# Kernel tuning notes

Measured on AMD Instinct MI355X. Metric: run time of the kernel, lower is better.

Reference implementation:

```python
import jax, jax.numpy as jnp
import numpy as np

B, T, I, H, O = 128, 2048, 128, 256, 128


def _lstm_step(h, c, x_t, wx, bx, wh, bh):
    # gates: [B, 4H], chunk order: input, forget, cell, output
    gates = x_t @ wx.T + bx + h @ wh.T + bh
    i_g, f_g, g_g, o_g = jnp.split(gates, 4, axis=1)
    i_t = jax.nn.sigmoid(i_g)
    f_t = jax.nn.sigmoid(f_g)
    g_t = jnp.tanh(g_g)
    o_t = jax.nn.sigmoid(o_g)
    cy = c * f_t + i_t * g_t
    hy = o_t * jnp.tanh(cy)
    return hy, cy


def _gru_step(h, x_t, wx, bx, wh, bh):
    # chunk order: reset, update, new
    x_g = x_t @ wx.T + bx
    h_g = h @ wh.T + bh
    x_r, x_z, x_n = jnp.split(x_g, 3, axis=1)
    h_r, h_z, h_n = jnp.split(h_g, 3, axis=1)
    r = jax.nn.sigmoid(x_r + h_r)
    z = jax.nn.sigmoid(x_z + h_z)
    n = jnp.tanh(x_n + r * h_n)
    return z * h + (1.0 - z) * n


def _run_direction(x_tbi, w1x, b1x, w1h, b1h, w2x, b2x, w2h, b2h):
    # x_tbi: [T, B, I]; returns final hidden of top cell [B, H]
    h1 = jnp.zeros((x_tbi.shape[1], H), x_tbi.dtype)
    c1 = jnp.zeros_like(h1)
    h2 = jnp.zeros_like(h1)

    def step(carry, x_t):
        h1, c1, h2 = carry
        h1, c1 = _lstm_step(h1, c1, x_t, w1x, b1x, w1h, b1h)
        h2 = _gru_step(h2, h1, w2x, b2x, w2h, b2h)
        return (h1, c1, h2), None

    (h1, c1, h2), _ = jax.lax.scan(step, (h1, c1, h2), x_tbi)
    return h2


def setup_inputs() -> dict:
    key = jax.random.key(0)
    ks = jax.random.split(key, 8)
    std1 = 1.0 / np.sqrt(H)
    u = lambda k, shape, s: jax.random.uniform(k, shape, jnp.float32, -s, s)
    x = jax.random.normal(ks[0], (B, T, I), jnp.float32)
    # Cell 1: LSTM(input=I, hidden=H)
    w1x = u(ks[1], (4 * H, I), std1)
    b1x = jnp.zeros((4 * H,), jnp.float32)
    w1h = u(ks[2], (4 * H, H), std1)
    b1h = jnp.zeros((4 * H,), jnp.float32)
    # Cell 2: GRU(input=H, hidden=H)
    w2x = u(ks[3], (3 * H, H), std1)
    b2x = jnp.zeros((3 * H,), jnp.float32)
    w2h = u(ks[4], (3 * H, H), std1)
    b2h = jnp.zeros((3 * H,), jnp.float32)
    # out_fc: Linear(2H -> O), kaiming-normal fan_in
    wo = jax.random.normal(ks[5], (O, 2 * H), jnp.float32) * np.sqrt(2.0 / (2 * H))
    bo = jnp.zeros((O,), jnp.float32)
    return {"x": x, "w1x": w1x, "b1x": b1x, "w1h": w1h, "b1h": b1h,
            "w2x": w2x, "b2x": b2x, "w2h": w2h, "b2h": b2h, "wo": wo, "bo": bo}


def reference(x, w1x, b1x, w1h, b1h, w2x, b2x, w2h, b2h, wo, bo):
    x_tbi = jnp.swapaxes(x, 0, 1)  # [T, B, I]
    h_fwd = _run_direction(x_tbi, w1x, b1x, w1h, b1h, w2x, b2x, w2h, b2h)
    h_bwd = _run_direction(x_tbi[::-1], w1x, b1x, w1h, b1h, w2x, b2x, w2h, b2h)
    h_cat = jnp.concatenate([h_fwd, h_bwd], axis=1)  # [B, 2H]
    return h_cat @ wo.T + bo  # [B, O]
```

## Files before the change

### kernel.cpp

```cpp
#include <hip/hip_runtime.h>

#define T_LEN 2048
#define I_DIM 128
#define H_DIM 256


#define XHI_OFF 0
#define XLO_OFF 8192
#define CRED_OFF 16384
#define HSTG_OFF 33280
#define LDS_BYTES 98304

typedef __attribute__((ext_vector_type(8))) short short8;
typedef __attribute__((ext_vector_type(16))) float f32x16;

__device__ __forceinline__ float sigmoidf_(float v) { return 1.f / (1.f + __expf(-v)); }
__device__ __forceinline__ float tanhf_fast(float v) {
    float t = __expf(-2.f * fabsf(v));
    float r = (1.f - t) / (1.f + t);
    return v < 0.f ? -r : r;
}
__device__ __forceinline__ unsigned short bf16_rne(float f) {
    unsigned u = __float_as_uint(f);
    return (unsigned short)((u + 0x7fffu + ((u >> 16) & 1u)) >> 16);
}
__device__ __forceinline__ void split2(float a, unsigned short& h, unsigned short& l) {
    h = bf16_rne(a);
    float hf = __uint_as_float(((unsigned)h) << 16);
    l = bf16_rne(a - hf);
}

__device__ __forceinline__ short8 ld_frag(const char* p) {
    union { unsigned long long u[2]; short8 s; } v;
    v.u[0] = __hip_atomic_load((const unsigned long long*)p,
                               __ATOMIC_RELAXED, __HIP_MEMORY_SCOPE_AGENT);
    v.u[1] = __hip_atomic_load((const unsigned long long*)(p + 8),
                               __ATOMIC_RELAXED, __HIP_MEMORY_SCOPE_AGENT);
    return v.s;
}

__device__ __forceinline__ void stage_x_fn(const float* __restrict__ x, char* smem_b,
                                           int b0, int teff, int tid) {
    int b = tid >> 3, cq = tid & 7;
    const float4* src = (const float4*)(x + ((size_t)(b0 + b) * T_LEN + teff) * I_DIM + cq * 16);
    float4 v0 = src[0], v1 = src[1], v2 = src[2], v3 = src[3];
    float f[16] = {v0.x, v0.y, v0.z, v0.w, v1.x, v1.y, v1.z, v1.w,
                   v2.x, v2.y, v2.z, v2.w, v3.x, v3.y, v3.z, v3.w};
    short8 H0, H1, L0, L1;
    #pragma unroll
    for (int e = 0; e < 8; ++e) {
        unsigned short h, l;
        split2(f[e], h, l);      H0[e] = (short)h; L0[e] = (short)l;
        split2(f[8 + e], h, l);  H1[e] = (short)h; L1[e] = (short)l;
    }
    char* base = smem_b + cq * 1024 + b * 16;
    *(short8*)(base + XHI_OFF)       = H0;
    *(short8*)(base + XHI_OFF + 512) = H1;
    *(short8*)(base + XLO_OFF)       = L0;
    *(short8*)(base + XLO_OFF + 512) = L1;
}

#define MFMA3(ac, ah, al, bh, bl)                                              \
    ac = __builtin_amdgcn_mfma_f32_32x32x16_bf16(ah, bh, ac, 0, 0, 0);         \
    ac = __builtin_amdgcn_mfma_f32_32x32x16_bf16(ah, bl, ac, 0, 0, 0);         \
    ac = __builtin_amdgcn_mfma_f32_32x32x16_bf16(al, bh, ac, 0, 0, 0);

#define ACCSEL(i) ((i & 3) == 0 ? acc0 : (i & 3) == 1 ? acc1 : (i & 3) == 2 ? acc2 : acc3)

__global__ __launch_bounds__(256, 1)
void brnn_persistent(const float* __restrict__ x,
                     const float* __restrict__ w1x, const float* __restrict__ b1x,
                     const float* __restrict__ w1h, const float* __restrict__ b1h,
                     const float* __restrict__ w2x, const float* __restrict__ b2x,
                     const float* __restrict__ w2h, const float* __restrict__ b2h,
                     int* flags, char* exgb, float* h2out)
{
    extern __shared__ char smem_b[];

    const int tid  = threadIdx.x;
    const int lane = tid & 63;
    const int wid  = tid >> 6;
    const int wg   = blockIdx.x;
    const int grp  = wg & 7;
    const int cu   = wg >> 3;
    const int dir  = grp >> 2;
    const int btile = grp & 3;
    const int b0   = btile * 32;

    const int nrow = lane & 31;
    const int jrow = nrow >> 2;
    const int q    = nrow & 3;
    const int half = lane >> 5;
    short8 BH[16], BL[16];
    {
        #pragma unroll
        for (int i = 0; i < 16; ++i) {
            short8 H, L;
            #pragma unroll
            for (int e = 0; e < 8; ++e) {
                int kk = i * 16 + half * 8 + e;
                float v = 0.f;
                if (wid == 0) {
                    if (i < 12) {
                        int k = kk;
                        int R = q * H_DIM + cu * 8 + jrow;
                        v = (k < I_DIM) ? w1x[R * I_DIM + k] : w1h[R * H_DIM + (k - I_DIM)];
                    }
                } else if (wid == 1) {
                    if (i < 12) {
                        int k = 192 + kk;
                        int R = q * H_DIM + cu * 8 + jrow;
                        v = w1h[R * H_DIM + (k - I_DIM)];
                    }
                } else if (wid == 2) {
                    if (q < 3) v = w2x[(q * H_DIM + cu * 8 + jrow) * H_DIM + kk];
                } else {
                    if (q == 0)      v = w2h[(0 * H_DIM + cu * 8 + jrow) * H_DIM + kk];
                    else if (q == 1) v = w2h[(1 * H_DIM + cu * 8 + jrow) * H_DIM + kk];
                    else if (q == 3) v = w2h[(2 * H_DIM + cu * 8 + jrow) * H_DIM + kk];
                }
                unsigned short hh, ll;
                split2(v, hh, ll);
                H[e] = (short)hh; L[e] = (short)ll;
            }
            BH[i] = H; BL[i] = L;
        }
    }

    const int bb = tid & 31;
    const int jj = tid >> 5;
    const float bi_ = b1x[0 * H_DIM + cu * 8 + jj] + b1h[0 * H_DIM + cu * 8 + jj];
    const float bf_ = b1x[1 * H_DIM + cu * 8 + jj] + b1h[1 * H_DIM + cu * 8 + jj];
    const float bg_ = b1x[2 * H_DIM + cu * 8 + jj] + b1h[2 * H_DIM + cu * 8 + jj];
    const float bo_ = b1x[3 * H_DIM + cu * 8 + jj] + b1h[3 * H_DIM + cu * 8 + jj];
    const float brz_r = b2x[0 * H_DIM + cu * 8 + jj] + b2h[0 * H_DIM + cu * 8 + jj];
    const float brz_z = b2x[1 * H_DIM + cu * 8 + jj] + b2h[1 * H_DIM + cu * 8 + jj];
    const float bnx_  = b2x[2 * H_DIM + cu * 8 + jj];
    const float bnh_  = b2h[2 * H_DIM + cu * 8 + jj];

    float c_reg = 0.f, h2_reg = 0.f;

    {
        char* p1 = exgb + (size_t)(1 * 8 + grp) * 65536;
        int off = (cu >> 1) * 1024 + (cu & 1) * 512;
        if (tid < 64) {
            __hip_atomic_store((unsigned long long*)(p1 + off + tid * 8), 0ull,
                               __ATOMIC_RELAXED, __HIP_MEMORY_SCOPE_AGENT);
            __hip_atomic_store((unsigned long long*)(p1 + 32768 + off + tid * 8), 0ull,
                               __ATOMIC_RELAXED, __HIP_MEMORY_SCOPE_AGENT);
        }
    }
    if (tid < 128) *(unsigned long long*)(smem_b + HSTG_OFF + 1024 + tid * 8) = 0ull;
    stage_x_fn(x, smem_b, b0, dir ? (T_LEN - 1) : 0, tid);
    __syncthreads();
    if (tid == 0)
        __hip_atomic_store(&flags[grp * 64 + cu], 1,
                           __ATOMIC_RELAXED, __HIP_MEMORY_SCOPE_AGENT);

    for (int s = 0; s <= T_LEN; ++s) {
        {
            int target = s + 1;
            if (tid < 64) {
                while (true) {
                    int v = (tid < 32)
                        ? __hip_atomic_load(&flags[grp * 64 + tid],
                                            __ATOMIC_RELAXED, __HIP_MEMORY_SCOPE_AGENT)
                        : 0x7fffffff;
                    if (__all(v >= target)) break;
                }
            }
            __syncthreads();
        }
        const char* exgR = exgb + (size_t)(((s + 1) & 1) * 8 + grp) * 65536;

        f32x16 acc0, acc1, acc2, acc3;
        #pragma unroll
        for (int r = 0; r < 16; ++r) { acc0[r] = 0.f; acc1[r] = 0.f; acc2[r] = 0.f; acc3[r] = 0.f; }

        if (wid == 0) {
            if (s < T_LEN) {
                short8 hA[4], lA[4];
                #pragma unroll
                for (int i = 0; i < 4; ++i) {
                    hA[i] = ld_frag(exgR + i * 1024 + lane * 16);
                    lA[i] = ld_frag(exgR + 32768 + i * 1024 + lane * 16);
                }
                #pragma unroll
                for (int i = 0; i < 8; ++i) {
                    short8 ah = *(const short8*)(smem_b + XHI_OFF + i * 1024 + lane * 16);
                    short8 al = *(const short8*)(smem_b + XLO_OFF + i * 1024 + lane * 16);
                    f32x16& ac = ACCSEL(i);
                    MFMA3(ac, ah, al, BH[i], BL[i]);
                }
                #pragma unroll
                for (int i = 0; i < 4; ++i) {
                    f32x16& ac = ACCSEL(8 + i);
                    MFMA3(ac, hA[i], lA[i], BH[8 + i], BL[8 + i]);
                }
            }
        } else if (wid == 1) {
            if (s < T_LEN) {
                short8 hA[12], lA[12];
                #pragma unroll
                for (int i = 0; i < 12; ++i) {
                    hA[i] = ld_frag(exgR + (4 + i) * 1024 + lane * 16);
                    lA[i] = ld_frag(exgR + 32768 + (4 + i) * 1024 + lane * 16);
                }
                #pragma unroll
                for (int i = 0; i < 12; ++i) {
                    f32x16& ac = ACCSEL(i);
                    MFMA3(ac, hA[i], lA[i], BH[i], BL[i]);
                }
            }
        } else {
            if (s >= 1) {
                const int sbase = (wid - 2) * 16;
                short8 hA[16], lA[16];
                #pragma unroll
                for (int i = 0; i < 16; ++i) {
                    hA[i] = ld_frag(exgR + (sbase + i) * 1024 + lane * 16);
                    lA[i] = ld_frag(exgR + 32768 + (sbase + i) * 1024 + lane * 16);
                }
                #pragma unroll
                for (int i = 0; i < 16; ++i) {
                    f32x16& ac = ACCSEL(i);
                    MFMA3(ac, hA[i], lA[i], BH[i], BL[i]);
                }
            }
        }
        {
            float* credw = (float*)(smem_b + CRED_OFF) + wid * 1056;
            #pragma unroll
            for (int r = 0; r < 16; ++r) {
                int b = (r & 3) + 8 * (r >> 2) + 4 * half;
                credw[nrow * 33 + b] = acc0[r] + acc1[r] + acc2[r] + acc3[r];
            }
        }
        __syncthreads();

        const float* cr = (const float*)(smem_b + CRED_OFF);
        #define CRD(w, g) cr[(w) * 1056 + (jj * 4 + (g)) * 33 + bb]
        if (s < T_LEN) {
            float gi = CRD(0, 0) + CRD(1, 0) + bi_;
            float gf = CRD(0, 1) + CRD(1, 1) + bf_;
            float gg = CRD(0, 2) + CRD(1, 2) + bg_;
            float go = CRD(0, 3) + CRD(1, 3) + bo_;
            float ig = sigmoidf_(gi), fg = sigmoidf_(gf);
            float cg = tanhf_fast(gg), og = sigmoidf_(go);
            c_reg = c_reg * fg + ig * cg;
            float h1v = og * tanhf_fast(c_reg);
            unsigned short h, l;
            split2(h1v, h, l);
            *(unsigned short*)(smem_b + HSTG_OFF + bb * 16 + jj * 2) = h;
            *(unsigned short*)(smem_b + HSTG_OFF + 512 + bb * 16 + jj * 2) = l;
        }
        if (s >= 1) {
            float rc = CRD(2, 0) + CRD(3, 0) + brz_r;
            float zc = CRD(2, 1) + CRD(3, 1) + brz_z;
            float xn = CRD(2, 2) + CRD(3, 2) + bnx_;
            float hn = CRD(2, 3) + CRD(3, 3) + bnh_;
            float rg = sigmoidf_(rc), zg = sigmoidf_(zc);
            float ng = tanhf_fast(xn + rg * hn);
            h2_reg = zg * h2_reg + (1.f - zg) * ng;
            if (s == T_LEN) {
                h2out[(size_t)(grp * 32 + bb) * H_DIM + cu * 8 + jj] = h2_reg;
            } else {
                unsigned short h, l;
                split2(h2_reg, h, l);
                *(unsigned short*)(smem_b + HSTG_OFF + 1024 + bb * 16 + jj * 2) = h;
                *(unsigned short*)(smem_b + HSTG_OFF + 1536 + bb * 16 + jj * 2) = l;
            }
        }
        #undef CRD
        __syncthreads();

        if (s == T_LEN) break;

        {
            char* exgW = exgb + (size_t)((s & 1) * 8 + grp) * 65536;
            unsigned long long v = *(const unsigned long long*)(smem_b + HSTG_OFF + tid * 8);
            int r = tid >> 6;
            int w = (tid & 63) * 8;
            int off = (r & 1) * 32768 + ((r >> 1) * 16 + (cu >> 1)) * 1024 + (cu & 1) * 512 + w;
            __hip_atomic_store((unsigned long long*)(exgW + off), v,
                               __ATOMIC_RELAXED, __HIP_MEMORY_SCOPE_AGENT);
        }
        __syncthreads();
        if (tid == 0)
            __hip_atomic_store(&flags[grp * 64 + cu], s + 2,
                               __ATOMIC_RELAXED, __HIP_MEMORY_SCOPE_AGENT);
        if (s + 1 < T_LEN)
            stage_x_fn(x, smem_b, b0, dir ? (T_LEN - 2 - s) : (s + 1), tid);
    }
}

__global__ __launch_bounds__(128)
void brnn_out(const float* __restrict__ h2out, const float* __restrict__ wo,
              const float* __restrict__ bo, float* __restrict__ out)
{
    __shared__ float hc[512];
    int b = blockIdx.x;
    int o = threadIdx.x;
    int btile = b >> 5, bi = b & 31;
    for (int k = threadIdx.x; k < 256; k += 128) {
        hc[k]       = h2out[((size_t)(btile)     * 32 + bi) * H_DIM + k];
        hc[256 + k] = h2out[((size_t)(4 + btile) * 32 + bi) * H_DIM + k];
    }
    __syncthreads();
    float acc = bo[o];
    const float4* w4 = (const float4*)&wo[(size_t)o * 512];
    #pragma unroll 8
    for (int k = 0; k < 128; ++k) {
        float4 w = w4[k];
        acc += w.x * hc[k * 4] + w.y * hc[k * 4 + 1] + w.z * hc[k * 4 + 2] + w.w * hc[k * 4 + 3];
    }
    out[b * 128 + o] = acc;
}

extern "C" void kernel_launch(void* const* d_in, const int* in_sizes, int n_in,
                              void* d_out, int out_size, void* d_ws, size_t ws_size,
                              hipStream_t stream) {
    const float* x   = (const float*)d_in[0];
    const float* w1x = (const float*)d_in[1];
    const float* b1x = (const float*)d_in[2];
    const float* w1h = (const float*)d_in[3];
    const float* b1h = (const float*)d_in[4];
    const float* w2x = (const float*)d_in[5];
    const float* b2x = (const float*)d_in[6];
    const float* w2h = (const float*)d_in[7];
    const float* b2h = (const float*)d_in[8];
    const float* wo  = (const float*)d_in[9];
    const float* bo  = (const float*)d_in[10];
    float* out = (float*)d_out;

    char* ws = (char*)d_ws;
    int* flags = (int*)ws;
    char* exgb = ws + 4096;
    float* h2out = (float*)(ws + 4096 + 1048576);

    hipMemsetAsync(flags, 0, 8 * 64 * sizeof(int), stream);

    size_t shmem = LDS_BYTES;
    hipFuncSetAttribute((const void*)brnn_persistent,
                        hipFuncAttributeMaxDynamicSharedMemorySize, (int)shmem);

    void* args[] = { (void*)&x, (void*)&w1x, (void*)&b1x, (void*)&w1h, (void*)&b1h,
                     (void*)&w2x, (void*)&b2x, (void*)&w2h, (void*)&b2h,
                     (void*)&flags, (void*)&exgb, (void*)&h2out };
    hipError_t err = hipLaunchCooperativeKernel((void*)brnn_persistent,
                                                dim3(256), dim3(256), args,
                                                (unsigned int)shmem, stream);
    if (err != hipSuccess) {
        brnn_persistent<<<dim3(256), dim3(256), shmem, stream>>>(
            x, w1x, b1x, w1h, b1h, w2x, b2x, w2h, b2h, flags, exgb, h2out);
    }

    brnn_out<<<dim3(128), dim3(128), 0, stream>>>(h2out, wo, bo, out);
}
```

Measured before the change: 13.01 ms.

## Decouple LSTM and GRU warp pairs with separate flags and intra-block barriers

Splits each block into an LSTM half and a GRU half. Each half has its own LDS spin barrier and its own global progress flag, so the GRU half can lag the LSTM by one step instead of both marching in lockstep under __syncthreads. Hidden states are written straight to the global exchange buffer from the pointwise threads, which removes the staging copy and an extra block barrier. The x input is prefetched two steps ahead into a triple buffer by one LSTM warp. The cost is extra polling of two flag arrays, spin barriers built on LDS atomics, and more complex ordering that could introduce races.

```diff
diff --git a/kernel.cpp b/kernel.cpp
--- a/kernel.cpp
+++ b/kernel.cpp
@@ -5,10 +5,9 @@
 #define H_DIM 256
 
 
-#define XHI_OFF 0
-#define XLO_OFF 8192
-#define CRED_OFF 16384
-#define HSTG_OFF 33280
+#define XB(p)    ((p) * 16384)
+#define CRED_OFF 49152
+#define BAR_OFF  66048
 #define LDS_BYTES 98304
 
 typedef __attribute__((ext_vector_type(8))) short short8;
@@ -29,7 +28,6 @@
     float hf = __uint_as_float(((unsigned)h) << 16);
     l = bf16_rne(a - hf);
 }
-
 __device__ __forceinline__ short8 ld_frag(const char* p) {
     union { unsigned long long u[2]; short8 s; } v;
     v.u[0] = __hip_atomic_load((const unsigned long long*)p,
@@ -38,10 +36,14 @@
                                __ATOMIC_RELAXED, __HIP_MEMORY_SCOPE_AGENT);
     return v.s;
 }
-
-__device__ __forceinline__ void stage_x_fn(const float* __restrict__ x, char* smem_b,
-                                           int b0, int teff, int tid) {
-    int b = tid >> 3, cq = tid & 7;
+__device__ __forceinline__ void pair_bar(int* c, int target) {
+    __threadfence_block();
+    __hip_atomic_fetch_add(c, 1, __ATOMIC_RELAXED, __HIP_MEMORY_SCOPE_WORKGROUP);
+    while (__hip_atomic_load(c, __ATOMIC_RELAXED, __HIP_MEMORY_SCOPE_WORKGROUP) < target) {}
+}
+
+__device__ __forceinline__ void stage_unit(const float* __restrict__ x, char* hi, char* lo,
+                                           int b0, int teff, int b, int cq) {
     const float4* src = (const float4*)(x + ((size_t)(b0 + b) * T_LEN + teff) * I_DIM + cq * 16);
     float4 v0 = src[0], v1 = src[1], v2 = src[2], v3 = src[3];
     float f[16] = {v0.x, v0.y, v0.z, v0.w, v1.x, v1.y, v1.z, v1.w,
@@ -53,11 +55,10 @@
         split2(f[e], h, l);      H0[e] = (short)h; L0[e] = (short)l;
         split2(f[8 + e], h, l);  H1[e] = (short)h; L1[e] = (short)l;
     }
-    char* base = smem_b + cq * 1024 + b * 16;
-    *(short8*)(base + XHI_OFF)       = H0;
-    *(short8*)(base + XHI_OFF + 512) = H1;
-    *(short8*)(base + XLO_OFF)       = L0;
-    *(short8*)(base + XLO_OFF + 512) = L1;
+    char* bh = hi + cq * 1024 + b * 16;
+    char* bl = lo + cq * 1024 + b * 16;
+    *(short8*)bh = H0; *(short8*)(bh + 512) = H1;
+    *(short8*)bl = L0; *(short8*)(bl + 512) = L1;
 }
 
 #define MFMA3(ac, ah, al, bh, bl)                                              \
@@ -127,105 +128,124 @@
         }
     }
 
-    const int bb = tid & 31;
-    const int jj = tid >> 5;
-    const float bi_ = b1x[0 * H_DIM + cu * 8 + jj] + b1h[0 * H_DIM + cu * 8 + jj];
-    const float bf_ = b1x[1 * H_DIM + cu * 8 + jj] + b1h[1 * H_DIM + cu * 8 + jj];
-    const float bg_ = b1x[2 * H_DIM + cu * 8 + jj] + b1h[2 * H_DIM + cu * 8 + jj];
-    const float bo_ = b1x[3 * H_DIM + cu * 8 + jj] + b1h[3 * H_DIM + cu * 8 + jj];
-    const float brz_r = b2x[0 * H_DIM + cu * 8 + jj] + b2h[0 * H_DIM + cu * 8 + jj];
-    const float brz_z = b2x[1 * H_DIM + cu * 8 + jj] + b2h[1 * H_DIM + cu * 8 + jj];
-    const float bnx_  = b2x[2 * H_DIM + cu * 8 + jj];
-    const float bnh_  = b2h[2 * H_DIM + cu * 8 + jj];
-
-    float c_reg = 0.f, h2_reg = 0.f;
-
+    const int tt  = (tid < 128) ? tid : (tid - 128);
+    const int bbn = tt & 31;
+    const int qn  = tt >> 5;
+    float biasA[2][4];
+    #pragma unroll
+    for (int e = 0; e < 2; ++e) {
+        int jg = cu * 8 + 2 * qn + e;
+        if (tid < 128) {
+            #pragma unroll
+            for (int g = 0; g < 4; ++g)
+                biasA[e][g] = b1x[g * H_DIM + jg] + b1h[g * H_DIM + jg];
+        } else {
+            biasA[e][0] = b2x[0 * H_DIM + jg] + b2h[0 * H_DIM + jg];
+            biasA[e][1] = b2x[1 * H_DIM + jg] + b2h[1 * H_DIM + jg];
+            biasA[e][2] = b2x[2 * H_DIM + jg];
+            biasA[e][3] = b2h[2 * H_DIM + jg];
+        }
+    }
+    float st[2] = {0.f, 0.f};
+
+    int* lstm_bar = (int*)(smem_b + BAR_OFF);
+    int* gru_bar  = (int*)(smem_b + BAR_OFF + 64);
+    int* h1f = flags + grp * 128;
+    int* h2f = flags + grp * 128 + 64;
+
+    if (tid < 2) *(int*)(smem_b + BAR_OFF + tid * 64) = 0;
     {
-        char* p1 = exgb + (size_t)(1 * 8 + grp) * 65536;
-        int off = (cu >> 1) * 1024 + (cu & 1) * 512;
-        if (tid < 64) {
-            __hip_atomic_store((unsigned long long*)(p1 + off + tid * 8), 0ull,
-                               __ATOMIC_RELAXED, __HIP_MEMORY_SCOPE_AGENT);
-            __hip_atomic_store((unsigned long long*)(p1 + 32768 + off + tid * 8), 0ull,
-                               __ATOMIC_RELAXED, __HIP_MEMORY_SCOPE_AGENT);
-        }
-    }
-    if (tid < 128) *(unsigned long long*)(smem_b + HSTG_OFF + 1024 + tid * 8) = 0ull;
-    stage_x_fn(x, smem_b, b0, dir ? (T_LEN - 1) : 0, tid);
+        char* p1 = exgb + (size_t)(8 + grp) * 65536;
+        int r = tid >> 6, w = (tid & 63) * 8;
+        int off = (r & 1) * 32768 + ((r >> 1) * 16 + (cu >> 1)) * 1024 + (cu & 1) * 512 + w;
+        __hip_atomic_store((unsigned long long*)(p1 + off), 0ull,
+                           __ATOMIC_RELAXED, __HIP_MEMORY_SCOPE_AGENT);
+    }
+    {
+        int b = tid >> 3, cq = tid & 7;
+        stage_unit(x, smem_b + XB(0), smem_b + XB(0) + 8192, b0, dir ? (T_LEN - 1) : 0, b, cq);
+        stage_unit(x, smem_b + XB(1), smem_b + XB(1) + 8192, b0, dir ? (T_LEN - 2) : 1, b, cq);
+    }
     __syncthreads();
-    if (tid == 0)
-        __hip_atomic_store(&flags[grp * 64 + cu], 1,
-                           __ATOMIC_RELAXED, __HIP_MEMORY_SCOPE_AGENT);
-
-    for (int s = 0; s <= T_LEN; ++s) {
+    if (tid == 0) {
+        __hip_atomic_store(&h1f[cu], 1, __ATOMIC_RELAXED, __HIP_MEMORY_SCOPE_AGENT);
+        __hip_atomic_store(&h2f[cu], 1, __ATOMIC_RELAXED, __HIP_MEMORY_SCOPE_AGENT);
+    }
+
+    for (int s = 0; s < T_LEN; ++s) {
         {
-            int target = s + 1;
-            if (tid < 64) {
-                while (true) {
-                    int v = (tid < 32)
-                        ? __hip_atomic_load(&flags[grp * 64 + tid],
-                                            __ATOMIC_RELAXED, __HIP_MEMORY_SCOPE_AGENT)
-                        : 0x7fffffff;
-                    if (__all(v >= target)) break;
-                }
-            }
-            __syncthreads();
-        }
-        const char* exgR = exgb + (size_t)(((s + 1) & 1) * 8 + grp) * 65536;
+            int t1 = (wid < 2) ? (s + 1) : (s + 2);
+            int t2 = (wid < 2) ? s : (s + 1);
+            const int* fp = (lane < 32) ? &h1f[lane] : &h2f[lane - 32];
+            int tgt = (lane < 32) ? t1 : t2;
+            while (true) {
+                int v = __hip_atomic_load(fp, __ATOMIC_RELAXED, __HIP_MEMORY_SCOPE_AGENT);
+                if (__all(v >= tgt)) break;
+            }
+        }
+        const char* exgPrev = exgb + (size_t)((((s + 1) & 1)) * 8 + grp) * 65536;
+        char*       exgCur  = exgb + (size_t)(((s & 1)) * 8 + grp) * 65536;
 
         f32x16 acc0, acc1, acc2, acc3;
         #pragma unroll
         for (int r = 0; r < 16; ++r) { acc0[r] = 0.f; acc1[r] = 0.f; acc2[r] = 0.f; acc3[r] = 0.f; }
 
         if (wid == 0) {
-            if (s < T_LEN) {
-                short8 hA[4], lA[4];
-                #pragma unroll
-                for (int i = 0; i < 4; ++i) {
-                    hA[i] = ld_frag(exgR + i * 1024 + lane * 16);
-                    lA[i] = ld_frag(exgR + 32768 + i * 1024 + lane * 16);
-                }
-                #pragma unroll
-                for (int i = 0; i < 8; ++i) {
-                    short8 ah = *(const short8*)(smem_b + XHI_OFF + i * 1024 + lane * 16);
-                    short8 al = *(const short8*)(smem_b + XLO_OFF + i * 1024 + lane * 16);
-                    f32x16& ac = ACCSEL(i);
-                    MFMA3(ac, ah, al, BH[i], BL[i]);
-                }
-                #pragma unroll
-                for (int i = 0; i < 4; ++i) {
-                    f32x16& ac = ACCSEL(8 + i);
-                    MFMA3(ac, hA[i], lA[i], BH[8 + i], BL[8 + i]);
-                }
+            short8 hA[4], lA[4];
+            #pragma unroll
+            for (int i = 0; i < 4; ++i) {
+                hA[i] = ld_frag(exgPrev + i * 1024 + lane * 16);
+                lA[i] = ld_frag(exgPrev + 32768 + i * 1024 + lane * 16);
+            }
+            const char* xh = smem_b + XB(s % 3);
+            const char* xl = xh + 8192;
+            #pragma unroll
+            for (int i = 0; i < 8; ++i) {
+                short8 ah = *(const short8*)(xh + i * 1024 + lane * 16);
+                short8 al = *(const short8*)(xl + i * 1024 + lane * 16);
+                f32x16& ac = ACCSEL(i);
+                MFMA3(ac, ah, al, BH[i], BL[i]);
+            }
+            #pragma unroll
+            for (int i = 0; i < 4; ++i) {
+                f32x16& ac = ACCSEL(8 + i);
+                MFMA3(ac, hA[i], lA[i], BH[8 + i], BL[8 + i]);
             }
         } else if (wid == 1) {
-            if (s < T_LEN) {
-                short8 hA[12], lA[12];
-                #pragma unroll
-                for (int i = 0; i < 12; ++i) {
-                    hA[i] = ld_frag(exgR + (4 + i) * 1024 + lane * 16);
-                    lA[i] = ld_frag(exgR + 32768 + (4 + i) * 1024 + lane * 16);
-                }
-                #pragma unroll
-                for (int i = 0; i < 12; ++i) {
-                    f32x16& ac = ACCSEL(i);
-                    MFMA3(ac, hA[i], lA[i], BH[i], BL[i]);
-                }
+            short8 hA[12], lA[12];
+            #pragma unroll
+            for (int i = 0; i < 12; ++i) {
+                hA[i] = ld_frag(exgPrev + (4 + i) * 1024 + lane * 16);
+                lA[i] = ld_frag(exgPrev + 32768 + (4 + i) * 1024 + lane * 16);
+            }
+            #pragma unroll
+            for (int i = 0; i < 12; ++i) {
+                f32x16& ac = ACCSEL(i);
+                MFMA3(ac, hA[i], lA[i], BH[i], BL[i]);
+            }
+        } else if (wid == 2) {
+            short8 hA[16], lA[16];
+            #pragma unroll
+            for (int i = 0; i < 16; ++i) {
+                hA[i] = ld_frag(exgCur + i * 1024 + lane * 16);
+                lA[i] = ld_frag(exgCur + 32768 + i * 1024 + lane * 16);
+            }
+            #pragma unroll
+            for (int i = 0; i < 16; ++i) {
+                f32x16& ac = ACCSEL(i);
+                MFMA3(ac, hA[i], lA[i], BH[i], BL[i]);
             }
         } else {
-            if (s >= 1) {
-                const int sbase = (wid - 2) * 16;
-                short8 hA[16], lA[16];
-                #pragma unroll
-                for (int i = 0; i < 16; ++i) {
-                    hA[i] = ld_frag(exgR + (sbase + i) * 1024 + lane * 16);
-                    lA[i] = ld_frag(exgR + 32768 + (sbase + i) * 1024 + lane * 16);
-                }
-                #pragma unroll
-                for (int i = 0; i < 16; ++i) {
-                    f32x16& ac = ACCSEL(i);
-                    MFMA3(ac, hA[i], lA[i], BH[i], BL[i]);
-                }
+            short8 hA[16], lA[16];
+            #pragma unroll
+            for (int i = 0; i < 16; ++i) {
+                hA[i] = ld_frag(exgPrev + (16 + i) * 1024 + lane * 16);
+                lA[i] = ld_frag(exgPrev + 32768 + (16 + i) * 1024 + lane * 16);
+            }
+            #pragma unroll
+            for (int i = 0; i < 16; ++i) {
+                f32x16& ac = ACCSEL(i);
+                MFMA3(ac, hA[i], lA[i], BH[i], BL[i]);
             }
         }
         {
@@ -236,61 +256,82 @@
                 credw[nrow * 33 + b] = acc0[r] + acc1[r] + acc2[r] + acc3[r];
             }
         }
-        __syncthreads();
+        int* bar = (wid < 2) ? lstm_bar : gru_bar;
+        pair_bar(bar, 128 * (2 * s + 1));
 
         const float* cr = (const float*)(smem_b + CRED_OFF);
-        #define CRD(w, g) cr[(w) * 1056 + (jj * 4 + (g)) * 33 + bb]
-        if (s < T_LEN) {
-            float gi = CRD(0, 0) + CRD(1, 0) + bi_;
-            float gf = CRD(0, 1) + CRD(1, 1) + bf_;
-            float gg = CRD(0, 2) + CRD(1, 2) + bg_;
-            float go = CRD(0, 3) + CRD(1, 3) + bo_;
-            float ig = sigmoidf_(gi), fg = sigmoidf_(gf);
-            float cg = tanhf_fast(gg), og = sigmoidf_(go);
-            c_reg = c_reg * fg + ig * cg;
-            float h1v = og * tanhf_fast(c_reg);
-            unsigned short h, l;
-            split2(h1v, h, l);
-            *(unsigned short*)(smem_b + HSTG_OFF + bb * 16 + jj * 2) = h;
-            *(unsigned short*)(smem_b + HSTG_OFF + 512 + bb * 16 + jj * 2) = l;
-        }
-        if (s >= 1) {
-            float rc = CRD(2, 0) + CRD(3, 0) + brz_r;
-            float zc = CRD(2, 1) + CRD(3, 1) + brz_z;
-            float xn = CRD(2, 2) + CRD(3, 2) + bnx_;
-            float hn = CRD(2, 3) + CRD(3, 3) + bnh_;
-            float rg = sigmoidf_(rc), zg = sigmoidf_(zc);
-            float ng = tanhf_fast(xn + rg * hn);
-            h2_reg = zg * h2_reg + (1.f - zg) * ng;
-            if (s == T_LEN) {
-                h2out[(size_t)(grp * 32 + bb) * H_DIM + cu * 8 + jj] = h2_reg;
+        #define CRD(w, jj, g) cr[(w) * 1056 + ((jj) * 4 + (g)) * 33 + bbn]
+        if (tid < 128) {
+            unsigned hi32 = 0, lo32 = 0;
+            #pragma unroll
+            for (int e = 0; e < 2; ++e) {
+                int jj = 2 * qn + e;
+                float gi = CRD(0, jj, 0) + CRD(1, jj, 0) + biasA[e][0];
+                float gf = CRD(0, jj, 1) + CRD(1, jj, 1) + biasA[e][1];
+                float gg = CRD(0, jj, 2) + CRD(1, jj, 2) + biasA[e][2];
+                float go = CRD(0, jj, 3) + CRD(1, jj, 3) + biasA[e][3];
+                float ig = sigmoidf_(gi), fg = sigmoidf_(gf);
+                float cg = tanhf_fast(gg), og = sigmoidf_(go);
+                st[e] = st[e] * fg + ig * cg;
+                float h1v = og * tanhf_fast(st[e]);
+                unsigned short h, l;
+                split2(h1v, h, l);
+                hi32 |= ((unsigned)h) << (16 * e);
+                lo32 |= ((unsigned)l) << (16 * e);
+            }
+            int off = (cu >> 1) * 1024 + (cu & 1) * 512 + bbn * 16 + qn * 4;
+            __hip_atomic_store((unsigned*)(exgCur + off), hi32,
+                               __ATOMIC_RELAXED, __HIP_MEMORY_SCOPE_AGENT);
+            __hip_atomic_store((unsigned*)(exgCur + 32768 + off), lo32,
+                               __ATOMIC_RELAXED, __HIP_MEMORY_SCOPE_AGENT);
+            asm volatile("s_waitcnt vmcnt(0)" ::: "memory");
+            pair_bar(bar, 128 * (2 * s + 2));
+            if (tid == 0)
+                __hip_atomic_store(&h1f[cu], s + 2, __ATOMIC_RELAXED, __HIP_MEMORY_SCOPE_AGENT);
+            if (wid == 1 && s + 2 < T_LEN) {
+                int teff = dir ? (T_LEN - 3 - s) : (s + 2);
+                char* xh = smem_b + XB((s + 2) % 3);
+                char* xl = xh + 8192;
+                int t2i = tid - 64;
+                #pragma unroll
+                for (int i = 0; i < 4; ++i) {
+                    int u = i * 64 + t2i;
+                    stage_unit(x, xh, xl, b0, teff, u >> 3, u & 7);
+                }
+            }
+        } else {
+            unsigned hi32 = 0, lo32 = 0;
+            #pragma unroll
+            for (int e = 0; e < 2; ++e) {
+                int jj = 2 * qn + e;
+                float rc = CRD(2, jj, 0) + CRD(3, jj, 0) + biasA[e][0];
+                float zc = CRD(2, jj, 1) + CRD(3, jj, 1) + biasA[e][1];
+                float xn = CRD(2, jj, 2) + CRD(3, jj, 2) + biasA[e][2];
+                float hn = CRD(2, jj, 3) + CRD(3, jj, 3) + biasA[e][3];
+                float rg = sigmoidf_(rc), zg = sigmoidf_(zc);
+                float ng = tanhf_fast(xn + rg * hn);
+                st[e] = zg * st[e] + (1.f - zg) * ng;
+                unsigned short h, l;
+                split2(st[e], h, l);
+                hi32 |= ((unsigned)h) << (16 * e);
+                lo32 |= ((unsigned)l) << (16 * e);
+            }
+            if (s == T_LEN - 1) {
+                h2out[(size_t)(grp * 32 + bbn) * H_DIM + cu * 8 + 2 * qn]     = st[0];
+                h2out[(size_t)(grp * 32 + bbn) * H_DIM + cu * 8 + 2 * qn + 1] = st[1];
             } else {
-                unsigned short h, l;
-                split2(h2_reg, h, l);
-                *(unsigned short*)(smem_b + HSTG_OFF + 1024 + bb * 16 + jj * 2) = h;
-                *(unsigned short*)(smem_b + HSTG_OFF + 1536 + bb * 16 + jj * 2) = l;
-            }
+                int off = 16384 + (cu >> 1) * 1024 + (cu & 1) * 512 + bbn * 16 + qn * 4;
+                __hip_atomic_store((unsigned*)(exgCur + off), hi32,
+                                   __ATOMIC_RELAXED, __HIP_MEMORY_SCOPE_AGENT);
+                __hip_atomic_store((unsigned*)(exgCur + 32768 + off), lo32,
+                                   __ATOMIC_RELAXED, __HIP_MEMORY_SCOPE_AGENT);
+            }
+            asm volatile("s_waitcnt vmcnt(0)" ::: "memory");
+            pair_bar(bar, 128 * (2 * s + 2));
+            if (tid == 128 && s < T_LEN - 1)
+                __hip_atomic_store(&h2f[cu], s + 2, __ATOMIC_RELAXED, __HIP_MEMORY_SCOPE_AGENT);
         }
         #undef CRD
-        __syncthreads();
-
-        if (s == T_LEN) break;
-
-        {
-            char* exgW = exgb + (size_t)((s & 1) * 8 + grp) * 65536;
-            unsigned long long v = *(const unsigned long long*)(smem_b + HSTG_OFF + tid * 8);
-            int r = tid >> 6;
-            int w = (tid & 63) * 8;
-            int off = (r & 1) * 32768 + ((r >> 1) * 16 + (cu >> 1)) * 1024 + (cu & 1) * 512 + w;
-            __hip_atomic_store((unsigned long long*)(exgW + off), v,
-                               __ATOMIC_RELAXED, __HIP_MEMORY_SCOPE_AGENT);
-        }
-        __syncthreads();
-        if (tid == 0)
-            __hip_atomic_store(&flags[grp * 64 + cu], s + 2,
-                               __ATOMIC_RELAXED, __HIP_MEMORY_SCOPE_AGENT);
-        if (s + 1 < T_LEN)
-            stage_x_fn(x, smem_b, b0, dir ? (T_LEN - 2 - s) : (s + 1), tid);
     }
 }
 
@@ -335,10 +376,10 @@
 
     char* ws = (char*)d_ws;
     int* flags = (int*)ws;
-    char* exgb = ws + 4096;
-    float* h2out = (float*)(ws + 4096 + 1048576);
-
-    hipMemsetAsync(flags, 0, 8 * 64 * sizeof(int), stream);
+    char* exgb = ws + 8192;
+    float* h2out = (float*)(ws + 8192 + 1048576);
+
+    hipMemsetAsync(flags, 0, 8 * 128 * sizeof(int), stream);
 
     size_t shmem = LDS_BYTES;
     hipFuncSetAttribute((const void*)brnn_persistent,
```

After: 18.76 ms. +44.2%, slower.
